# Optimization experiments

Hardware: AMD Instinct MI355X
Metric: run time of the kernel (lower is better)

## Reference

```python
import jax, jax.numpy as jnp
import numpy as np

N, D, H, E, C = 10000, 256, 512, 320000, 1  # nodes, feature_dim, nhid, edges, nclass


def setup_inputs() -> dict:
    key = jax.random.key(0)
    ks = jax.random.split(key, 8)
    x = jax.random.normal(ks[0], (N, D), jnp.float32)
    edge_src = jax.random.randint(ks[1], (E,), 0, N, jnp.int32)
    edge_dst = jax.random.randint(ks[2], (E,), 0, N, jnp.int32)
    # adjacency values of a row-normalized A (mean aggregation); ~1/avg_degree scale
    edge_val = jax.random.uniform(ks[3], (E,), jnp.float32) / 32.0
    W_conv = jax.random.normal(ks[4], (2 * D, H), jnp.float32) / np.sqrt(2 * D)
    b_conv = jnp.zeros((H,), jnp.float32)
    W1 = jax.random.normal(ks[5], (H, H), jnp.float32) / np.sqrt(H)
    b1 = jnp.zeros((H,), jnp.float32)
    prelu_a = jnp.full((H,), 0.25, jnp.float32)  # PReLU per-channel slope (torch init 0.25)
    W2 = jax.random.normal(ks[6], (H, C), jnp.float32) / np.sqrt(H)
    b2 = jnp.zeros((C,), jnp.float32)
    return dict(x=x, edge_src=edge_src, edge_dst=edge_dst, edge_val=edge_val,
                W_conv=W_conv, b_conv=b_conv, W1=W1, b1=b1,
                prelu_a=prelu_a, W2=W2, b2=b2)


def reference(x, edge_src, edge_dst, edge_val, W_conv, b_conv, W1, b1, prelu_a, W2, b2):
    # MeanAggregator: agg = spmm(A, x) with A given as (dst, src, val) edge list
    msgs = x[edge_src] * edge_val[:, None]                         # [E, D] gather + scale
    agg = jax.ops.segment_sum(msgs, edge_dst, num_segments=x.shape[0])  # [N, D]
    # GraphConv: concat(self, agg) -> linear -> ReLU
    cat = jnp.concatenate([x, agg], axis=-1)                       # [N, 2D]
    h = jax.nn.relu(cat @ W_conv + b_conv)                         # [N, H]
    # classifier: Linear -> PReLU -> Linear, then view(-1)
    z = h @ W1 + b1                                                # [N, H]
    z = jnp.where(z > 0, z, prelu_a * z)                           # PReLU(nhid)
    pred = (z @ W2 + b2).reshape(-1)                               # [N * nclass]
    return pred
```

## Files before the change

### kernel.cpp

```cpp
#include <hip/hip_runtime.h>
#include <hip/hip_bf16.h>

#define N_NODES 10000
#define M_PAD   10112
#define DIM     256
#define HID     512
#define KDIM    512
#define N_EDGE  320000
#define ELL_W   128

typedef __attribute__((ext_vector_type(4))) float  f32x4;
typedef __attribute__((ext_vector_type(8))) __bf16 bf16x8;

__device__ __forceinline__ unsigned short f2bf(float f) {
    union { float f; unsigned int u; } v; v.f = f;
    unsigned int r = v.u + 0x7FFFu + ((v.u >> 16) & 1u);
    return (unsigned short)(r >> 16);
}
__device__ __forceinline__ float bf2f(unsigned short u) {
    union { unsigned int i; float f; } v; v.i = ((unsigned int)u) << 16;
    return v.f;
}

__device__ __forceinline__ void gload16(const void* g, void* l) {
    __builtin_amdgcn_global_load_lds(
        (const __attribute__((address_space(1))) void*)g,
        (__attribute__((address_space(3))) void*)l, 16, 0, 0);
}

__global__ void k_zero(int* __restrict__ deg) {
    int i = blockIdx.x * 256 + threadIdx.x;
    if (i < 10240) deg[i] = 0;
}

__device__ __forceinline__ void wtrans(const float* __restrict__ W,
                                       unsigned short* __restrict__ Wt,
                                       int tb, float (*tile)[65]) {
    const int t  = threadIdx.x;
    const int kb = (tb >> 3) * 64, nb = (tb & 7) * 64;
    const int r    = t >> 2;
    const int cseg = (t & 3) * 16;
    const float* src = W + (size_t)(kb + r) * 512 + nb + cseg;
    #pragma unroll
    for (int j = 0; j < 4; ++j)
        *(f32x4*)&tile[r][cseg + 4 * j] = *(const f32x4*)(src + 4 * j);
    __syncthreads();
    unsigned short* dst = Wt + (size_t)(nb + r) * 512 + kb + cseg;
    #pragma unroll
    for (int j = 0; j < 4; ++j) {
        ushort4 o;
        o.x = f2bf(tile[cseg + 4 * j + 0][r]);
        o.y = f2bf(tile[cseg + 4 * j + 1][r]);
        o.z = f2bf(tile[cseg + 4 * j + 2][r]);
        o.w = f2bf(tile[cseg + 4 * j + 3][r]);
        *(ushort4*)(dst + 4 * j) = o;
    }
}

__global__ void k_prep(const int* __restrict__ esrc, const int* __restrict__ edst,
                       const float* __restrict__ eval,
                       int* __restrict__ deg, int2* __restrict__ ell,
                       const float* __restrict__ x, unsigned short* __restrict__ cat,
                       const float* __restrict__ Wc, unsigned short* __restrict__ Wct,
                       const float* __restrict__ W1, unsigned short* __restrict__ W1t) {
    __shared__ float tile[64][65];
    int b = blockIdx.x;
    if (b < 1250) {
        int e = b * 256 + threadIdx.x;
        if (e < N_EDGE) {
            int d = edst[e];
            int slot = atomicAdd(&deg[d], 1);
            if (slot < ELL_W)
                ell[(size_t)d * ELL_W + slot] = make_int2(esrc[e], __float_as_int(eval[e]));
        }
    } else if (b < 3750) {
        int t  = (b - 1250) * 256 + threadIdx.x;
        int n  = t >> 6;
        int c4 = (t & 63) * 4;
        f32x4 v = *(const f32x4*)(x + (size_t)n * DIM + c4);
        ushort4 o;
        o.x = f2bf(v.x); o.y = f2bf(v.y); o.z = f2bf(v.z); o.w = f2bf(v.w);
        *(ushort4*)(cat + (size_t)n * 2 * DIM + c4) = o;
    } else if (b < 3814) {
        wtrans(Wc, Wct, b - 3750, tile);
    } else {
        wtrans(W1, W1t, b - 3814, tile);
    }
}

__global__ void k_agg(const int* __restrict__ deg, const int2* __restrict__ ell,
                      unsigned short* __restrict__ cat) {
    int wid  = (blockIdx.x * blockDim.x + threadIdx.x) >> 6;
    int lane = threadIdx.x & 63;
    if (wid >= N_NODES) return;
    int cnt = deg[wid];
    if (cnt > ELL_W) cnt = ELL_W;
    const int2* row = ell + (size_t)wid * ELL_W;
    int c4 = lane * 4;
    f32x4 a0 = {0.f,0.f,0.f,0.f}, a1 = a0, a2 = a0, a3 = a0;
    f32x4 a4 = a0, a5 = a0, a6 = a0, a7 = a0;
    for (int base = 0; base < cnt; base += 64) {
        int m = cnt - base;
        if (m > 64) m = 64;
        int2 my = make_int2(0, 0);
        if (lane < m) my = row[base + lane];
        int j = 0;
        for (; j + 8 <= m; j += 8) {
            int   s0 = __builtin_amdgcn_readlane(my.x, j);
            float v0 = __int_as_float(__builtin_amdgcn_readlane(my.y, j));
            int   s1 = __builtin_amdgcn_readlane(my.x, j + 1);
            float v1 = __int_as_float(__builtin_amdgcn_readlane(my.y, j + 1));
            int   s2 = __builtin_amdgcn_readlane(my.x, j + 2);
            float v2 = __int_as_float(__builtin_amdgcn_readlane(my.y, j + 2));
            int   s3 = __builtin_amdgcn_readlane(my.x, j + 3);
            float v3 = __int_as_float(__builtin_amdgcn_readlane(my.y, j + 3));
            int   s4 = __builtin_amdgcn_readlane(my.x, j + 4);
            float v4 = __int_as_float(__builtin_amdgcn_readlane(my.y, j + 4));
            int   s5 = __builtin_amdgcn_readlane(my.x, j + 5);
            float v5 = __int_as_float(__builtin_amdgcn_readlane(my.y, j + 5));
            int   s6 = __builtin_amdgcn_readlane(my.x, j + 6);
            float v6 = __int_as_float(__builtin_amdgcn_readlane(my.y, j + 6));
            int   s7 = __builtin_amdgcn_readlane(my.x, j + 7);
            float v7 = __int_as_float(__builtin_amdgcn_readlane(my.y, j + 7));
            ushort4 q0 = *(const ushort4*)(cat + (size_t)s0 * 2 * DIM + c4);
            ushort4 q1 = *(const ushort4*)(cat + (size_t)s1 * 2 * DIM + c4);
            ushort4 q2 = *(const ushort4*)(cat + (size_t)s2 * 2 * DIM + c4);
            ushort4 q3 = *(const ushort4*)(cat + (size_t)s3 * 2 * DIM + c4);
            ushort4 q4 = *(const ushort4*)(cat + (size_t)s4 * 2 * DIM + c4);
            ushort4 q5 = *(const ushort4*)(cat + (size_t)s5 * 2 * DIM + c4);
            ushort4 q6 = *(const ushort4*)(cat + (size_t)s6 * 2 * DIM + c4);
            ushort4 q7 = *(const ushort4*)(cat + (size_t)s7 * 2 * DIM + c4);
            a0.x += v0 * bf2f(q0.x); a0.y += v0 * bf2f(q0.y);
            a0.z += v0 * bf2f(q0.z); a0.w += v0 * bf2f(q0.w);
            a1.x += v1 * bf2f(q1.x); a1.y += v1 * bf2f(q1.y);
            a1.z += v1 * bf2f(q1.z); a1.w += v1 * bf2f(q1.w);
            a2.x += v2 * bf2f(q2.x); a2.y += v2 * bf2f(q2.y);
            a2.z += v2 * bf2f(q2.z); a2.w += v2 * bf2f(q2.w);
            a3.x += v3 * bf2f(q3.x); a3.y += v3 * bf2f(q3.y);
            a3.z += v3 * bf2f(q3.z); a3.w += v3 * bf2f(q3.w);
            a4.x += v4 * bf2f(q4.x); a4.y += v4 * bf2f(q4.y);
            a4.z += v4 * bf2f(q4.z); a4.w += v4 * bf2f(q4.w);
            a5.x += v5 * bf2f(q5.x); a5.y += v5 * bf2f(q5.y);
            a5.z += v5 * bf2f(q5.z); a5.w += v5 * bf2f(q5.w);
            a6.x += v6 * bf2f(q6.x); a6.y += v6 * bf2f(q6.y);
            a6.z += v6 * bf2f(q6.z); a6.w += v6 * bf2f(q6.w);
            a7.x += v7 * bf2f(q7.x); a7.y += v7 * bf2f(q7.y);
            a7.z += v7 * bf2f(q7.z); a7.w += v7 * bf2f(q7.w);
        }
        for (; j < m; ++j) {
            int   s0 = __builtin_amdgcn_readlane(my.x, j);
            float v0 = __int_as_float(__builtin_amdgcn_readlane(my.y, j));
            ushort4 q0 = *(const ushort4*)(cat + (size_t)s0 * 2 * DIM + c4);
            a0.x += v0 * bf2f(q0.x); a0.y += v0 * bf2f(q0.y);
            a0.z += v0 * bf2f(q0.z); a0.w += v0 * bf2f(q0.w);
        }
    }
    ushort4 o;
    o.x = f2bf(((a0.x + a1.x) + (a2.x + a3.x)) + ((a4.x + a5.x) + (a6.x + a7.x)));
    o.y = f2bf(((a0.y + a1.y) + (a2.y + a3.y)) + ((a4.y + a5.y) + (a6.y + a7.y)));
    o.z = f2bf(((a0.z + a1.z) + (a2.z + a3.z)) + ((a4.z + a5.z) + (a6.z + a7.z)));
    o.w = f2bf(((a0.w + a1.w) + (a2.w + a3.w)) + ((a4.w + a5.w) + (a6.w + a7.w)));
    *(ushort4*)(cat + (size_t)wid * 2 * DIM + DIM + c4) = o;
}

#define STAGE(buf, kt) { \
    _Pragma("unroll") \
    for (int i = 0; i < 4; ++i) { \
        gload16(pA + (size_t)i * 8 * KDIM + (kt) * 64, &As[buf][ldsbase + i * 512]); \
        gload16(pB + (size_t)i * 8 * KDIM + (kt) * 64, &Bs[buf][ldsbase + i * 512]); \
    } }

template <int MODE>
__global__ __launch_bounds__(256)
void k_gemm128(const unsigned short* __restrict__ A,
               const unsigned short* __restrict__ Bt,
               const float* __restrict__ bias,
               const float* __restrict__ pa,
               const float* __restrict__ w2,
               unsigned short* __restrict__ hout,
               float* __restrict__ part) {
    __shared__ unsigned short As[2][128 * 64];
    __shared__ unsigned short Bs[2][128 * 64];

    const int t    = threadIdx.x;
    const int lane = t & 63;
    const int w    = t >> 6;
    const int wr   = w >> 1, wc = w & 1;
    const int tn   = blockIdx.x & 3;
    const int tm   = blockIdx.x >> 2;
    const int gm0  = tm * 128, gn0 = tn * 128;

    const int srow = w * 32 + (lane >> 3);
    const int lc   = (lane & 7) ^ (lane >> 3);
    const unsigned short* pA = A  + (size_t)(gm0 + srow) * KDIM + lc * 8;
    const unsigned short* pB = Bt + (size_t)(gn0 + srow) * KDIM + lc * 8;
    const int ldsbase = w * 2048;

    const int r15 = lane & 15;
    const int hi  = lane >> 4;
    const int x7  = r15 & 7;

    f32x4 acc[4][4] = {};

    STAGE(0, 0);
    __syncthreads();

    #pragma unroll
    for (int ks = 0; ks < 8; ++ks) {
        const int cur = ks & 1;
        if (ks < 7) STAGE(cur ^ 1, ks + 1);
        #pragma unroll
        for (int kk = 0; kk < 2; ++kk) {
            const int pc = ((kk * 4 + hi) ^ x7) * 8;
            bf16x8 af[4], bf[4];
            #pragma unroll
            for (int m = 0; m < 4; ++m)
                af[m] = *(const bf16x8*)&As[cur][(wr * 64 + m * 16 + r15) * 64 + pc];
            #pragma unroll
            for (int n = 0; n < 4; ++n)
                bf[n] = *(const bf16x8*)&Bs[cur][(wc * 64 + n * 16 + r15) * 64 + pc];
            #pragma unroll
            for (int m = 0; m < 4; ++m)
                #pragma unroll
                for (int n = 0; n < 4; ++n)
                    acc[m][n] = __builtin_amdgcn_mfma_f32_16x16x32_bf16(af[m], bf[n], acc[m][n], 0, 0, 0);
        }
        if (ks < 7) __syncthreads();
    }

    const int rq = lane >> 4;
    if (MODE == 0) {
        #pragma unroll
        for (int n = 0; n < 4; ++n) {
            int c = gn0 + wc * 64 + n * 16 + r15;
            float b = bias[c];
            #pragma unroll
            for (int m = 0; m < 4; ++m) {
                #pragma unroll
                for (int i = 0; i < 4; ++i) {
                    int row = gm0 + wr * 64 + m * 16 + rq * 4 + i;
                    float v = acc[m][n][i] + b;
                    v = v > 0.f ? v : 0.f;
                    hout[(size_t)row * HID + c] = f2bf(v);
                }
            }
        }
    } else {
        float rsum[4][4] = {};
        #pragma unroll
        for (int n = 0; n < 4; ++n) {
            int c = gn0 + wc * 64 + n * 16 + r15;
            float b = bias[c];
            float a = pa[c];
            float wv = w2[c];
            #pragma unroll
            for (int m = 0; m < 4; ++m)
                #pragma unroll
                for (int i = 0; i < 4; ++i) {
                    float v = acc[m][n][i] + b;
                    v = v > 0.f ? v : a * v;
                    rsum[m][i] += v * wv;
                }
        }
        #pragma unroll
        for (int m = 0; m < 4; ++m)
            #pragma unroll
            for (int i = 0; i < 4; ++i) {
                float s = rsum[m][i];
                s += __shfl_xor(s, 1);
                s += __shfl_xor(s, 2);
                s += __shfl_xor(s, 4);
                s += __shfl_xor(s, 8);
                if (r15 == 0) {
                    int row = gm0 + wr * 64 + m * 16 + rq * 4 + i;
                    part[(size_t)(tn * 2 + wc) * M_PAD + row] = s;
                }
            }
    }
}

__global__ void k_vout(const float* __restrict__ part, const float* __restrict__ b2,
                       float* __restrict__ pred) {
    int row = blockIdx.x * blockDim.x + threadIdx.x;
    if (row >= N_NODES) return;
    float s = b2[0];
    #pragma unroll
    for (int j = 0; j < 8; ++j) s += part[(size_t)j * M_PAD + row];
    pred[row] = s;
}

extern "C" void kernel_launch(void* const* d_in, const int* in_sizes, int n_in,
                              void* d_out, int out_size, void* d_ws, size_t ws_size,
                              hipStream_t stream) {
    const float* x    = (const float*)d_in[0];
    const int*   esrc = (const int*)  d_in[1];
    const int*   edst = (const int*)  d_in[2];
    const float* eval = (const float*)d_in[3];
    const float* Wc   = (const float*)d_in[4];
    const float* bc   = (const float*)d_in[5];
    const float* W1   = (const float*)d_in[6];
    const float* b1   = (const float*)d_in[7];
    const float* pa   = (const float*)d_in[8];
    const float* W2   = (const float*)d_in[9];
    const float* b2   = (const float*)d_in[10];
    float* pred = (float*)d_out;

    char* w = (char*)d_ws;
    int*            deg   = (int*)w;
    int2*           ell   = (int2*)(w + 40960);
    unsigned short* cat   = (unsigned short*)(w + 10526720);
    unsigned short* Wct   = (unsigned short*)(w + 20881408);
    unsigned short* W1t   = (unsigned short*)(w + 21405696);
    unsigned short* h     = (unsigned short*)(w + 21929984);
    float*          partb = (float*)(w + 32284672);

    k_zero<<<40, 256, 0, stream>>>(deg);

    k_prep<<<3878, 256, 0, stream>>>(esrc, edst, eval, deg, ell, x, cat, Wc, Wct, W1, W1t);

    k_agg<<<(N_NODES * 64 + 255) / 256, 256, 0, stream>>>(deg, ell, cat);

    k_gemm128<0><<<316, 256, 0, stream>>>(cat, Wct, bc, nullptr, nullptr, h, nullptr);
    k_gemm128<1><<<316, 256, 0, stream>>>(h, W1t, b1, pa, W2, nullptr, partb);

    k_vout<<<(N_NODES + 255) / 256, 256, 0, stream>>>(partb, b2, pred);
}
```

Baseline: 88.10 us.

## Fuse both GEMMs and output reduction into one persistent kernel with grid barriers

Merges the two GEMM launches and the final reduction kernel into a single persistent kernel of 256 blocks. The blocks loop over the 316 tiles and synchronise through atomic-counter grid barriers. This removes two kernel launch gaps and their tail effects. In exchange, 256 blocks each take one or two tiles, which gives load imbalance (60 blocks do two tiles). The spin barrier relies on all 256 blocks being co-resident.

```diff
diff --git a/kernel.cpp b/kernel.cpp
--- a/kernel.cpp
+++ b/kernel.cpp
@@ -8,6 +8,8 @@
 #define KDIM    512
 #define N_EDGE  320000
 #define ELL_W   128
+#define NTILES  316
+#define NBLK    256
 
 typedef __attribute__((ext_vector_type(4))) float  f32x4;
 typedef __attribute__((ext_vector_type(8))) __bf16 bf16x8;
@@ -28,9 +30,10 @@
         (__attribute__((address_space(3))) void*)l, 16, 0, 0);
 }
 
-__global__ void k_zero(int* __restrict__ deg) {
+__global__ void k_zero(int* __restrict__ deg, int* __restrict__ cnt) {
     int i = blockIdx.x * 256 + threadIdx.x;
     if (i < 10240) deg[i] = 0;
+    if (i < 8)     cnt[i] = 0;
 }
 
 __device__ __forceinline__ void wtrans(const float* __restrict__ W,
@@ -171,23 +174,24 @@
     } }
 
 template <int MODE>
-__global__ __launch_bounds__(256)
-void k_gemm128(const unsigned short* __restrict__ A,
-               const unsigned short* __restrict__ Bt,
-               const float* __restrict__ bias,
-               const float* __restrict__ pa,
-               const float* __restrict__ w2,
-               unsigned short* __restrict__ hout,
-               float* __restrict__ part) {
-    __shared__ unsigned short As[2][128 * 64];
-    __shared__ unsigned short Bs[2][128 * 64];
+__device__ void gemm_tile(int tile,
+                          const unsigned short* __restrict__ A,
+                          const unsigned short* __restrict__ Bt,
+                          const float* __restrict__ bias,
+                          const float* __restrict__ pa,
+                          const float* __restrict__ w2,
+                          unsigned short* __restrict__ hout,
+                          float* __restrict__ part,
+                          unsigned short (*As)[8192],
+                          unsigned short (*Bs)[8192]) {
+    __syncthreads();
 
     const int t    = threadIdx.x;
     const int lane = t & 63;
     const int w    = t >> 6;
     const int wr   = w >> 1, wc = w & 1;
-    const int tn   = blockIdx.x & 3;
-    const int tm   = blockIdx.x >> 2;
+    const int tn   = tile & 3;
+    const int tm   = tile >> 2;
     const int gm0  = tm * 128, gn0 = tn * 128;
 
     const int srow = w * 32 + (lane >> 3);
@@ -279,14 +283,44 @@
     }
 }
 
-__global__ void k_vout(const float* __restrict__ part, const float* __restrict__ b2,
-                       float* __restrict__ pred) {
-    int row = blockIdx.x * blockDim.x + threadIdx.x;
-    if (row >= N_NODES) return;
-    float s = b2[0];
-    #pragma unroll
-    for (int j = 0; j < 8; ++j) s += part[(size_t)j * M_PAD + row];
-    pred[row] = s;
+__device__ __forceinline__ void gbar(int* cnt) {
+    __threadfence();
+    __syncthreads();
+    if (threadIdx.x == 0) {
+        __hip_atomic_fetch_add(cnt, 1, __ATOMIC_ACQ_REL, __HIP_MEMORY_SCOPE_AGENT);
+        while (__hip_atomic_load(cnt, __ATOMIC_ACQUIRE, __HIP_MEMORY_SCOPE_AGENT) < NBLK)
+            __builtin_amdgcn_s_sleep(8);
+    }
+    __syncthreads();
+}
+
+__global__ __launch_bounds__(256)
+void k_mlp(const unsigned short* __restrict__ cat,
+           const unsigned short* __restrict__ Wct, const float* __restrict__ bc,
+           const unsigned short* __restrict__ W1t, const float* __restrict__ b1,
+           const float* __restrict__ pa, const float* __restrict__ W2,
+           const float* __restrict__ b2,
+           unsigned short* __restrict__ h, float* __restrict__ part,
+           float* __restrict__ pred, int* __restrict__ cnt) {
+    __shared__ unsigned short As[2][8192];
+    __shared__ unsigned short Bs[2][8192];
+    const int bid = blockIdx.x;
+
+    for (int tile = bid; tile < NTILES; tile += NBLK)
+        gemm_tile<0>(tile, cat, Wct, bc, nullptr, nullptr, h, nullptr, As, Bs);
+    gbar(&cnt[0]);
+
+    for (int tile = bid; tile < NTILES; tile += NBLK)
+        gemm_tile<1>(tile, h, W1t, b1, pa, W2, nullptr, part, As, Bs);
+    gbar(&cnt[1]);
+
+    int row = bid * 256 + threadIdx.x;
+    if (row < N_NODES) {
+        float s = b2[0];
+        #pragma unroll
+        for (int j = 0; j < 8; ++j) s += part[(size_t)j * M_PAD + row];
+        pred[row] = s;
+    }
 }
 
 extern "C" void kernel_launch(void* const* d_in, const int* in_sizes, int n_in,
@@ -313,15 +347,14 @@
     unsigned short* W1t   = (unsigned short*)(w + 21405696);
     unsigned short* h     = (unsigned short*)(w + 21929984);
     float*          partb = (float*)(w + 32284672);
-
-    k_zero<<<40, 256, 0, stream>>>(deg);
+    int*            cnt   = (int*)(w + 32608256);
+
+    k_zero<<<41, 256, 0, stream>>>(deg, cnt);
 
     k_prep<<<3878, 256, 0, stream>>>(esrc, edst, eval, deg, ell, x, cat, Wc, Wct, W1, W1t);
 
     k_agg<<<(N_NODES * 64 + 255) / 256, 256, 0, stream>>>(deg, ell, cat);
 
-    k_gemm128<0><<<316, 256, 0, stream>>>(cat, Wct, bc, nullptr, nullptr, h, nullptr);
-    k_gemm128<1><<<316, 256, 0, stream>>>(h, W1t, b1, pa, W2, nullptr, partb);
-
-    k_vout<<<(N_NODES + 255) / 256, 256, 0, stream>>>(partb, b2, pred);
-}
+    k_mlp<<<NBLK, 256, 0, stream>>>(cat, Wct, bc, W1t, b1, pa, W2, b2,
+                                    h, partb, pred, cnt);
+}
```

New measurement: 227.3 us. +158.0%, slower.
